# Kernel tuning notes

Hardware: AMD Instinct MI355X
Metric: run time of the kernel (lower is better)

Reference implementation:

```python
import jax, jax.numpy as jnp
import numpy as np

B, T, C, H = 16, 2048, 1024, 128  # batch, seq_len (BLOCK_SIZE), EMBEDDING_SIZE, head_size


def setup_inputs() -> dict:
    key = jax.random.key(0)
    kx, kq, kk, kv = jax.random.split(key, 4)
    x = jax.random.normal(kx, (B, T, C), dtype=jnp.float32)
    Wq = jax.random.normal(kq, (C, H), dtype=jnp.float32) * (C ** -0.5)
    Wk = jax.random.normal(kk, (C, H), dtype=jnp.float32) * (C ** -0.5)
    Wv = jax.random.normal(kv, (C, H), dtype=jnp.float32) * (C ** -0.5)
    return {"x": x, "Wq": Wq, "Wk": Wk, "Wv": Wv}


def reference(x, Wq, Wk, Wv):
    # Single-head causal self-attention (dropout in eval mode -> identity).
    q = jnp.einsum('btc,ch->bth', x, Wq)
    k = jnp.einsum('btc,ch->bth', x, Wk)
    v = jnp.einsum('btc,ch->bth', x, Wv)
    scale = k.shape[-1] ** -0.5
    wei = jnp.einsum('bqh,bkh->bqk', q, k) * scale  # [B, T, T]
    # causal mask: position q attends to k <= q (tril == 1)
    causal = jnp.tril(jnp.ones((T, T), dtype=bool))
    wei = jnp.where(causal[None, :, :], wei, -jnp.inf)
    wei = jax.nn.softmax(wei, axis=-1)
    out = jnp.einsum('bqk,bkh->bqh', wei, v)  # [B, T, H]
    return out
```

## Files before the change

### kernel.cpp

```cpp
#include <hip/hip_runtime.h>
#include <hip/hip_bf16.h>
#include <stdint.h>


typedef __bf16 bf16x8 __attribute__((ext_vector_type(8)));
typedef __bf16 bf16x4 __attribute__((ext_vector_type(4)));
typedef float  f32x4  __attribute__((ext_vector_type(4)));
typedef uint32_t u32;

#define MFMA16(a, b, c) __builtin_amdgcn_mfma_f32_16x16x32_bf16((a), (b), (c), 0, 0, 0)
#define LOG2E 1.4426950408889634f

static __device__ __forceinline__ float exp2fast(float x) { return __builtin_exp2f(x); }

static __device__ __forceinline__ bf16x4 pack4(float4 a) {
  bf16x4 r;
  r[0] = (__bf16)a.x; r[1] = (__bf16)a.y; r[2] = (__bf16)a.z; r[3] = (__bf16)a.w;
  return r;
}

static __device__ __forceinline__ u32 pkbf16(float a, float b) {
  union { __bf16 h[2]; u32 u; } t;
  t.h[0] = (__bf16)a; t.h[1] = (__bf16)b;
  return t.u;
}

__global__ __launch_bounds__(256) void k_build_wt(
    const float* __restrict__ Wq, const float* __restrict__ Wk,
    const float* __restrict__ Wv, __bf16* __restrict__ WtB)
{
  __shared__ float tile[32][33];
  const int tx = threadIdx.x, ty = threadIdx.y;
  const int c0 = blockIdx.x * 32, h0 = blockIdx.y * 32, w = blockIdx.z;
  const float* W = (w == 0) ? Wq : (w == 1) ? Wk : Wv;
  const float s = (w == 0) ? 0.08838834764831843f : 1.0f;
#pragma unroll
  for (int i = 0; i < 4; ++i)
    tile[ty + i * 8][tx] = W[(size_t)(c0 + ty + i * 8) * 128 + h0 + tx];
  __syncthreads();
#pragma unroll
  for (int i = 0; i < 4; ++i) {
    const int n = w * 128 + h0 + ty + i * 8;
    WtB[(size_t)blockIdx.x * 12288 + (size_t)n * 32 + tx] =
        (__bf16)(tile[tx][ty + i * 8] * s);
  }
}

__global__ __launch_bounds__(512, 4) void k_proj(
    const float* __restrict__ x, const __bf16* __restrict__ WtB,
    __bf16* __restrict__ QT, __bf16* __restrict__ KT, __bf16* __restrict__ VT2)
{
  const int tid  = threadIdx.x;
  const int lane = tid & 63, wid = tid >> 6;
  const int lr = lane & 15, g = lane >> 4;
  const int m0 = blockIdx.x * 64;

  __shared__ __bf16 As[2][64][32];

  const int srow = tid >> 3;
  const int sc4  = (tid & 7) * 4;
  char* AsB = (char*)As;
  const int wbyte = (srow * 64 + sc4 * 2) ^ (((srow >> 1) & 3) << 4);
  const float* xrow = x + (size_t)(m0 + srow) * 1024 + sc4;

  const int nbase = wid * 48;
  const __bf16* wB = WtB + (size_t)(nbase + lr) * 32 + g * 8;

  f32x4 acc[4][3] = {};

  float4 xreg = *(const float4*)(xrow);
  bf16x8 bcur[3], bnext[3];
#pragma unroll
  for (int j = 0; j < 3; ++j)
    bcur[j] = *(const bf16x8*)(wB + (size_t)j * 512);

  for (int kt = 0; kt < 32; ++kt) {
    const int buf = kt & 1;
    *(bf16x4*)(AsB + buf * 4096 + wbyte) = pack4(xreg);
    if (kt < 31)
      xreg = *(const float4*)(xrow + (kt + 1) * 32);
    asm volatile("s_waitcnt lgkmcnt(0)\n\ts_barrier" ::: "memory");

    bf16x8 af[4];
#pragma unroll
    for (int i = 0; i < 4; ++i) {
      const int row = i * 16 + lr;
      af[i] = *(const bf16x8*)(AsB + buf * 4096 +
                               (row * 64 + ((g * 16) ^ (((row >> 1) & 3) << 4))));
    }
    if (kt < 31) {
      const __bf16* wn = wB + (size_t)(kt + 1) * 12288;
#pragma unroll
      for (int j = 0; j < 3; ++j)
        bnext[j] = *(const bf16x8*)(wn + (size_t)j * 512);
    }
#pragma unroll
    for (int j = 0; j < 3; ++j)
#pragma unroll
      for (int i = 0; i < 4; ++i)
        acc[i][j] = MFMA16(af[i], bcur[j], acc[i][j]);
#pragma unroll
    for (int j = 0; j < 3; ++j) bcur[j] = bnext[j];
  }

  const int b = m0 >> 11;
#pragma unroll
  for (int j = 0; j < 3; ++j) {
    const int n = nbase + j * 16 + lr;
#pragma unroll
    for (int i = 0; i < 4; ++i) {
      const int m = m0 + i * 16 + g * 4;
      const int tt = m & 2047;
#pragma unroll
      for (int rr = 0; rr < 4; ++rr) {
        const float v = acc[i][j][rr];
        if (n < 128) {
          QT[(size_t)b * 262144 + (size_t)((tt + rr) >> 4) * 2048 +
             (n >> 5) * 512 + ((tt + rr) & 15) * 32 + (n & 31)] = (__bf16)v;
        } else if (n < 256) {
          const int nk = n - 128;
          KT[(size_t)b * 262144 + (size_t)((tt + rr) >> 4) * 2048 +
             (nk >> 5) * 512 + ((tt + rr) & 15) * 32 + (nk & 31)] = (__bf16)v;
        } else {
          const int d = n - 256, kv = tt + rr;
          VT2[(size_t)b * 262144 + (size_t)(d >> 4) * 32768 +
              (kv >> 5) * 512 + (d & 15) * 32 + (kv & 31)] = (__bf16)v;
        }
      }
    }
  }
}

__global__ __launch_bounds__(256, 2) void k_attn(
    const __bf16* __restrict__ QT, const __bf16* __restrict__ KT,
    const __bf16* __restrict__ VT2, float* __restrict__ out)
{
  const int tid  = threadIdx.x;
  const int lane = tid & 63, wid = tid >> 6;
  const int lr = lane & 15, g = lane >> 4;
  const int b  = blockIdx.y;
  const int q0 = (int)(gridDim.x - 1 - blockIdx.x) * 16;

  __shared__ float Lo[4][16][132];
  __shared__ float Lml[4][16][2];

  const __bf16* QTb = QT  + (size_t)b * 262144;
  const __bf16* KTb = KT  + (size_t)b * 262144;
  const __bf16* VTb = VT2 + (size_t)b * 262144;
  const int fo = lr * 32 + g * 8;

  bf16x8 qf[4];
#pragma unroll
  for (int d4 = 0; d4 < 4; ++d4)
    qf[d4] = *(const bf16x8*)(QTb + (size_t)(q0 >> 4) * 2048 + d4 * 512 + fo);

  f32x4 o[8] = {};
  float m = -1e30f, l = 0.0f;

  const int ntiles = (q0 >> 5) + 1;
  bf16x8 kf0[4], kf1[4];
  if (wid < ntiles) {
    const __bf16* kp = KTb + (size_t)wid * 4096 + fo;
#pragma unroll
    for (int d4 = 0; d4 < 4; ++d4) {
      kf0[d4] = *(const bf16x8*)(kp + d4 * 512);
      kf1[d4] = *(const bf16x8*)(kp + 2048 + d4 * 512);
    }
  }

  for (int t = wid; t < ntiles; t += 4) {
    const int kv0 = t << 5;
    bf16x8 vf[8];
#pragma unroll
    for (int dt = 0; dt < 8; ++dt)
      vf[dt] = *(const bf16x8*)(VTb + (size_t)dt * 32768 + (size_t)(kv0 >> 5) * 512 + fo);
    bf16x8 kf0n[4], kf1n[4];
    const int tn = t + 4;
    if (tn < ntiles) {
      const __bf16* kp = KTb + (size_t)tn * 4096 + fo;
#pragma unroll
      for (int d4 = 0; d4 < 4; ++d4) {
        kf0n[d4] = *(const bf16x8*)(kp + d4 * 512);
        kf1n[d4] = *(const bf16x8*)(kp + 2048 + d4 * 512);
      }
    }

    f32x4 s0 = {}, s1 = {};
#pragma unroll
    for (int d4 = 0; d4 < 4; ++d4) {
      s0 = MFMA16(kf0[d4], qf[d4], s0);
      s1 = MFMA16(kf1[d4], qf[d4], s1);
    }

    if (kv0 + 31 > q0) {
      const int qrow = q0 + lr;
#pragma unroll
      for (int rr = 0; rr < 4; ++rr) {
        if (kv0 + g * 4 + rr > qrow)      s0[rr] = -1e30f;
        if (kv0 + 16 + g * 4 + rr > qrow) s1[rr] = -1e30f;
      }
    }
    float mx = fmaxf(fmaxf(fmaxf(s0[0], s0[1]), fmaxf(s0[2], s0[3])),
                     fmaxf(fmaxf(s1[0], s1[1]), fmaxf(s1[2], s1[3])));
    mx = fmaxf(mx, __shfl_xor(mx, 16));
    mx = fmaxf(mx, __shfl_xor(mx, 32));
    const float mnew = fmaxf(m, mx);
    const float al = exp2fast((m - mnew) * LOG2E);
    float p[8];
#pragma unroll
    for (int rr = 0; rr < 4; ++rr) {
      p[rr]     = exp2fast((s0[rr] - mnew) * LOG2E);
      p[4 + rr] = exp2fast((s1[rr] - mnew) * LOG2E);
    }
    float ps = ((p[0] + p[1]) + (p[2] + p[3])) + ((p[4] + p[5]) + (p[6] + p[7]));
    ps += __shfl_xor(ps, 16);
    ps += __shfl_xor(ps, 32);
    l = l * al + ps;
    m = mnew;

    const u32 c0 = pkbf16(p[0], p[1]), c1 = pkbf16(p[2], p[3]);
    const u32 c2 = pkbf16(p[4], p[5]), c3 = pkbf16(p[6], p[7]);
    const int srcA = (lr + ((g & 1) << 5)) << 2;
    const u32 lo0 = (u32)__builtin_amdgcn_ds_bpermute(srcA,      (int)c0);
    const u32 lo1 = (u32)__builtin_amdgcn_ds_bpermute(srcA,      (int)c1);
    const u32 hi0 = (u32)__builtin_amdgcn_ds_bpermute(srcA,      (int)c2);
    const u32 hi1 = (u32)__builtin_amdgcn_ds_bpermute(srcA,      (int)c3);
    const u32 lo2 = (u32)__builtin_amdgcn_ds_bpermute(srcA + 64, (int)c0);
    const u32 lo3 = (u32)__builtin_amdgcn_ds_bpermute(srcA + 64, (int)c1);
    const u32 hi2 = (u32)__builtin_amdgcn_ds_bpermute(srcA + 64, (int)c2);
    const u32 hi3 = (u32)__builtin_amdgcn_ds_bpermute(srcA + 64, (int)c3);
    const bool hi = (g & 2) != 0;
    union { u32 u[4]; bf16x8 v; } pu;
    pu.u[0] = hi ? hi0 : lo0;
    pu.u[1] = hi ? hi1 : lo1;
    pu.u[2] = hi ? hi2 : lo2;
    pu.u[3] = hi ? hi3 : lo3;
    const bf16x8 pb = pu.v;

#pragma unroll
    for (int dt = 0; dt < 8; ++dt) {
#pragma unroll
      for (int rr = 0; rr < 4; ++rr) o[dt][rr] *= al;
    }
#pragma unroll
    for (int dt = 0; dt < 8; ++dt)
      o[dt] = MFMA16(vf[dt], pb, o[dt]);

#pragma unroll
    for (int d4 = 0; d4 < 4; ++d4) { kf0[d4] = kf0n[d4]; kf1[d4] = kf1n[d4]; }
  }

#pragma unroll
  for (int dt = 0; dt < 8; ++dt)
    *(f32x4*)&Lo[wid][lr][dt * 16 + g * 4] = o[dt];
  if (lane < 16) { Lml[wid][lr][0] = m; Lml[wid][lr][1] = l; }
  __syncthreads();

  const int row = tid >> 4, cg = tid & 15;
  float mw[4], lw[4];
#pragma unroll
  for (int w = 0; w < 4; ++w) { mw[w] = Lml[w][row][0]; lw[w] = Lml[w][row][1]; }
  const float M = fmaxf(fmaxf(mw[0], mw[1]), fmaxf(mw[2], mw[3]));
  float wt[4], L = 0.0f;
#pragma unroll
  for (int w = 0; w < 4; ++w) { wt[w] = exp2fast((mw[w] - M) * LOG2E); L += lw[w] * wt[w]; }
  const float inv = 1.0f / L;
  f32x4 acc0 = {}, acc1 = {};
#pragma unroll
  for (int w = 0; w < 4; ++w) {
    const f32x4 v0 = *(const f32x4*)&Lo[w][row][cg * 8];
    const f32x4 v1 = *(const f32x4*)&Lo[w][row][cg * 8 + 4];
    acc0 += v0 * wt[w];
    acc1 += v1 * wt[w];
  }
  float* orow = out + ((size_t)b * 2048 + q0 + row) * 128 + cg * 8;
  *(f32x4*)orow       = acc0 * inv;
  *(f32x4*)(orow + 4) = acc1 * inv;
}

extern "C" void kernel_launch(void* const* d_in, const int* in_sizes, int n_in,
                              void* d_out, int out_size, void* d_ws, size_t ws_size,
                              hipStream_t stream) {
  const float* x  = (const float*)d_in[0];
  const float* Wq = (const float*)d_in[1];
  const float* Wk = (const float*)d_in[2];
  const float* Wv = (const float*)d_in[3];
  float* out = (float*)d_out;

  char* ws = (char*)d_ws;
  __bf16* WtB = (__bf16*)(ws);
  __bf16* QT  = (__bf16*)(ws + 786432);
  __bf16* KT  = (__bf16*)(ws + 9175040);
  __bf16* VT2 = (__bf16*)(ws + 17563648);

  k_build_wt<<<dim3(32, 4, 3), dim3(32, 8), 0, stream>>>(Wq, Wk, Wv, WtB);
  k_proj    <<<dim3(512),      dim3(512),   0, stream>>>(x, WtB, QT, KT, VT2);
  k_attn    <<<dim3(128, 16),  dim3(256),   0, stream>>>(QT, KT, VT2, out);
}
```

Baseline: 313.4 us.

## Raise attention occupancy, halve LDS merge buffer, skip redundant rescale, set MFMA priority

Several changes land together in the attention kernel. The launch bound goes from 2 to 4 blocks per CU, and the LDS staging buffer is halved by merging the output in two passes over 64 columns each. The grid is flattened so that batch varies fastest within each query-block index, and the online-softmax rescale of the accumulator is skipped when no lane's max increases. MFMA sections are wrapped in s_setprio to favour matrix issue. The tighter register budget may cause spills, and the two-pass merge adds an extra barrier.

```diff
diff --git a/kernel.cpp b/kernel.cpp
--- a/kernel.cpp
+++ b/kernel.cpp
@@ -131,17 +131,19 @@
   }
 }
 
-__global__ __launch_bounds__(256, 2) void k_attn(
+__global__ __launch_bounds__(256, 4) void k_attn(
     const __bf16* __restrict__ QT, const __bf16* __restrict__ KT,
     const __bf16* __restrict__ VT2, float* __restrict__ out)
 {
   const int tid  = threadIdx.x;
   const int lane = tid & 63, wid = tid >> 6;
   const int lr = lane & 15, g = lane >> 4;
-  const int b  = blockIdx.y;
-  const int q0 = (int)(gridDim.x - 1 - blockIdx.x) * 16;
-
-  __shared__ float Lo[4][16][132];
+  const int flat = blockIdx.x;
+  const int b    = flat & 15;
+  const int qblk = flat >> 4;
+  const int q0   = (127 - qblk) << 4;
+
+  __shared__ float Lo[4][16][68];
   __shared__ float Lml[4][16][2];
 
   const __bf16* QTb = QT  + (size_t)b * 262144;
@@ -186,11 +188,13 @@
     }
 
     f32x4 s0 = {}, s1 = {};
+    __builtin_amdgcn_s_setprio(1);
 #pragma unroll
     for (int d4 = 0; d4 < 4; ++d4) {
       s0 = MFMA16(kf0[d4], qf[d4], s0);
       s1 = MFMA16(kf1[d4], qf[d4], s1);
     }
+    __builtin_amdgcn_s_setprio(0);
 
     if (kv0 + 31 > q0) {
       const int qrow = q0 + lr;
@@ -204,19 +208,28 @@
                      fmaxf(fmaxf(s1[0], s1[1]), fmaxf(s1[2], s1[3])));
     mx = fmaxf(mx, __shfl_xor(mx, 16));
     mx = fmaxf(mx, __shfl_xor(mx, 32));
-    const float mnew = fmaxf(m, mx);
-    const float al = exp2fast((m - mnew) * LOG2E);
+
+    float al = 1.0f;
+    if (!__all(mx <= m)) {
+      const float mnew = fmaxf(m, mx);
+      al = exp2fast((m - mnew) * LOG2E);
+      m = mnew;
+#pragma unroll
+      for (int dt = 0; dt < 8; ++dt) {
+#pragma unroll
+        for (int rr = 0; rr < 4; ++rr) o[dt][rr] *= al;
+      }
+    }
     float p[8];
 #pragma unroll
     for (int rr = 0; rr < 4; ++rr) {
-      p[rr]     = exp2fast((s0[rr] - mnew) * LOG2E);
-      p[4 + rr] = exp2fast((s1[rr] - mnew) * LOG2E);
+      p[rr]     = exp2fast((s0[rr] - m) * LOG2E);
+      p[4 + rr] = exp2fast((s1[rr] - m) * LOG2E);
     }
     float ps = ((p[0] + p[1]) + (p[2] + p[3])) + ((p[4] + p[5]) + (p[6] + p[7]));
     ps += __shfl_xor(ps, 16);
     ps += __shfl_xor(ps, 32);
     l = l * al + ps;
-    m = mnew;
 
     const u32 c0 = pkbf16(p[0], p[1]), c1 = pkbf16(p[2], p[3]);
     const u32 c2 = pkbf16(p[4], p[5]), c3 = pkbf16(p[6], p[7]);
@@ -237,23 +250,20 @@
     pu.u[3] = hi ? hi3 : lo3;
     const bf16x8 pb = pu.v;
 
-#pragma unroll
-    for (int dt = 0; dt < 8; ++dt) {
-#pragma unroll
-      for (int rr = 0; rr < 4; ++rr) o[dt][rr] *= al;
-    }
+    __builtin_amdgcn_s_setprio(1);
 #pragma unroll
     for (int dt = 0; dt < 8; ++dt)
       o[dt] = MFMA16(vf[dt], pb, o[dt]);
+    __builtin_amdgcn_s_setprio(0);
 
 #pragma unroll
     for (int d4 = 0; d4 < 4; ++d4) { kf0[d4] = kf0n[d4]; kf1[d4] = kf1n[d4]; }
   }
 
-#pragma unroll
-  for (int dt = 0; dt < 8; ++dt)
+  if (lane < 16) { Lml[wid][lr][0] = m; Lml[wid][lr][1] = l; }
+#pragma unroll
+  for (int dt = 0; dt < 4; ++dt)
     *(f32x4*)&Lo[wid][lr][dt * 16 + g * 4] = o[dt];
-  if (lane < 16) { Lml[wid][lr][0] = m; Lml[wid][lr][1] = l; }
   __syncthreads();
 
   const int row = tid >> 4, cg = tid & 15;
@@ -265,17 +275,25 @@
 #pragma unroll
   for (int w = 0; w < 4; ++w) { wt[w] = exp2fast((mw[w] - M) * LOG2E); L += lw[w] * wt[w]; }
   const float inv = 1.0f / L;
-  f32x4 acc0 = {}, acc1 = {};
-#pragma unroll
-  for (int w = 0; w < 4; ++w) {
-    const f32x4 v0 = *(const f32x4*)&Lo[w][row][cg * 8];
-    const f32x4 v1 = *(const f32x4*)&Lo[w][row][cg * 8 + 4];
-    acc0 += v0 * wt[w];
-    acc1 += v1 * wt[w];
-  }
-  float* orow = out + ((size_t)b * 2048 + q0 + row) * 128 + cg * 8;
-  *(f32x4*)orow       = acc0 * inv;
-  *(f32x4*)(orow + 4) = acc1 * inv;
+  float* orow = out + ((size_t)b * 2048 + q0 + row) * 128 + cg * 4;
+
+  f32x4 a0 = {};
+#pragma unroll
+  for (int w = 0; w < 4; ++w)
+    a0 += (*(const f32x4*)&Lo[w][row][cg * 4]) * wt[w];
+  *(f32x4*)orow = a0 * inv;
+  __syncthreads();
+
+#pragma unroll
+  for (int dt = 4; dt < 8; ++dt)
+    *(f32x4*)&Lo[wid][lr][(dt - 4) * 16 + g * 4] = o[dt];
+  __syncthreads();
+
+  f32x4 a1 = {};
+#pragma unroll
+  for (int w = 0; w < 4; ++w)
+    a1 += (*(const f32x4*)&Lo[w][row][cg * 4]) * wt[w];
+  *(f32x4*)(orow + 64) = a1 * inv;
 }
 
 extern "C" void kernel_launch(void* const* d_in, const int* in_sizes, int n_in,
@@ -295,5 +313,5 @@
 
   k_build_wt<<<dim3(32, 4, 3), dim3(32, 8), 0, stream>>>(Wq, Wk, Wv, WtB);
   k_proj    <<<dim3(512),      dim3(512),   0, stream>>>(x, WtB, QT, KT, VT2);
-  k_attn    <<<dim3(128, 16),  dim3(256),   0, stream>>>(QT, KT, VT2, out);
-}
+  k_attn    <<<dim3(2048),     dim3(256),   0, stream>>>(QT, KT, VT2, out);
+}
```

New measurement: 389.3 us. 1.24x slower.
